# Performance work log

Hardware: AMD Instinct MI355X
Metric: run time of the kernel (lower is better)

## Reference

```python
import jax, jax.numpy as jnp
import numpy as np
import math

D_MODEL = 1024
H = 16
D_K = D_MODEL // H          # 64
D_HALF = D_MODEL // 2       # 512
DH = D_HALF // H            # 32 (half head dim for q/k)
B, S = 2, 1024
LAMBDA_INIT = 0.8 - 0.6 * math.exp(-0.3 * (1 - 1))  # layer_index=1 -> 0.2


def setup_inputs() -> dict:
    key = jax.random.key(0)
    ks = jax.random.split(key, 20)
    def lin(kk, fan_in, fan_out):
        lim = 1.0 / math.sqrt(fan_in)
        kw, kb = jax.random.split(kk)
        W = jax.random.uniform(kw, (fan_in, fan_out), jnp.float32, -lim, lim)
        b = jax.random.uniform(kb, (fan_out,), jnp.float32, -lim, lim)
        return W, b
    Wq1, bq1 = lin(ks[0], D_MODEL, D_HALF)
    Wq2, bq2 = lin(ks[1], D_MODEL, D_HALF)
    Wk1, bk1 = lin(ks[2], D_MODEL, D_HALF)
    Wk2, bk2 = lin(ks[3], D_MODEL, D_HALF)
    Wv, bv = lin(ks[4], D_MODEL, D_MODEL)
    Wo, bo = lin(ks[5], D_MODEL, D_MODEL)
    q = jax.random.normal(ks[6], (B, S, D_MODEL), jnp.float32)
    k = jax.random.normal(ks[7], (B, S, D_MODEL), jnp.float32)
    v = jax.random.normal(ks[8], (B, S, D_MODEL), jnp.float32)
    # causal 0/1 mask, already 4-D [B,1,S,S]
    mask = jnp.broadcast_to(jnp.tril(jnp.ones((S, S), jnp.int32)), (B, 1, S, S))
    # small random lambda scalars (torch inits to 0 -> degenerate gradients)
    lq1 = jax.random.normal(ks[9], (1,), jnp.float32) * 0.1
    lk1 = jax.random.normal(ks[10], (1,), jnp.float32) * 0.1
    lq2 = jax.random.normal(ks[11], (1,), jnp.float32) * 0.1
    lk2 = jax.random.normal(ks[12], (1,), jnp.float32) * 0.1
    return dict(q=q, k=k, v=v, mask=mask,
                Wq1=Wq1, bq1=bq1, Wq2=Wq2, bq2=bq2,
                Wk1=Wk1, bk1=bk1, Wk2=Wk2, bk2=bk2,
                Wv=Wv, bv=bv, Wo=Wo, bo=bo,
                lq1=lq1, lk1=lk1, lq2=lq2, lk2=lk2)


def reference(q, k, v, mask, Wq1, bq1, Wq2, bq2, Wk1, bk1, Wk2, bk2,
              Wv, bv, Wo, bo, lq1, lk1, lq2, lk2):
    b, sq, _ = q.shape
    sk = k.shape[1]
    # projections, reshaped to [B, S, H, head_dim]
    q1 = (q @ Wq1 + bq1).reshape(b, sq, H, DH)
    q2 = (q @ Wq2 + bq2).reshape(b, sq, H, DH)
    k1 = (k @ Wk1 + bk1).reshape(b, sk, H, DH)
    k2 = (k @ Wk2 + bk2).reshape(b, sk, H, DH)
    vv = (v @ Wv + bv).reshape(b, sk, H, D_K)
    lam = jnp.exp(lq1 * lk1) - jnp.exp(lq2 * lk2) + LAMBDA_INIT  # shape (1,)
    scale = 1.0 / math.sqrt(D_K)
    s1 = jnp.einsum('bqhd,bkhd->bhqk', q1, k1) * scale
    s2 = jnp.einsum('bqhd,bkhd->bhqk', q2, k2) * scale
    neg = jnp.float32(-1e9)
    keep = mask != 0  # [B,1,Sq,Sk], broadcasts over heads
    s1 = jnp.where(keep, s1, neg)
    s2 = jnp.where(keep, s2, neg)
    a1 = jax.nn.softmax(s1, axis=-1)
    a2 = jax.nn.softmax(s2, axis=-1)
    diff = a1 - lam[0] * a2  # dropout p=0.0 -> identity
    out = jnp.einsum('bhqk,bkhd->bqhd', diff, vv).reshape(b, sq, D_MODEL)
    return out @ Wo + bo
```

## Files before the change

### kernel.cpp

```cpp
#include <hip/hip_runtime.h>
#include <hip/hip_bf16.h>
#include <cstdint>
#include <cstddef>

typedef __attribute__((ext_vector_type(8))) short short8;
typedef __attribute__((ext_vector_type(4))) float floatx4;

#define B_ 2
#define S_ 1024
#define H_ 16
#define DM_ 1024
#define DHALF_ 512
#define DH_ 32
#define DK_ 64
#define LAMBDA_INIT_ 0.2f
#define SCALE_ 0.125f
#define M_INIT_ -1.0e4f
#define MASK_NEG_ -1.0e9f

static __device__ __forceinline__ unsigned short f2bf(float f) {
  uint32_t u = __float_as_uint(f);
  uint32_t r = (u + 0x7fffu + ((u >> 16) & 1u)) >> 16;
  return (unsigned short)r;
}

static __device__ __forceinline__ uint32_t pkbf(float a, float b) {
  __hip_bfloat162 h = __float22bfloat162_rn(make_float2(a, b));
  return *reinterpret_cast<uint32_t*>(&h);
}

static __device__ __forceinline__ void gload16(const void* g, void* l) {
  __builtin_amdgcn_global_load_lds(
      (const __attribute__((address_space(1))) uint32_t*)g,
      (__attribute__((address_space(3))) uint32_t*)l, 16, 0, 0);
}

__global__ __launch_bounds__(256) void prep_kernel(
    const float* __restrict__ q, const float* __restrict__ k, const float* __restrict__ v,
    const float* __restrict__ Wq1, const float* __restrict__ Wq2,
    const float* __restrict__ Wk1, const float* __restrict__ Wk2,
    const float* __restrict__ Wv, const float* __restrict__ Wo,
    const float* __restrict__ bq1, const float* __restrict__ bq2,
    const float* __restrict__ bk1, const float* __restrict__ bk2,
    unsigned short* __restrict__ WqT, unsigned short* __restrict__ WkT,
    unsigned short* __restrict__ WvT, unsigned short* __restrict__ WoT,
    unsigned short* __restrict__ qbf, unsigned short* __restrict__ kbf,
    unsigned short* __restrict__ vbf,
    float* __restrict__ biasQ, float* __restrict__ biasK)
{
  __shared__ float tile[64][65];
  const int bid = blockIdx.x;
  const int tid = threadIdx.x;
  if (bid < 1024) {
    const float* W; unsigned short* WT; int ncols, n_off, local;
    if (bid < 128)      { W = Wq1; WT = WqT; ncols = 512;  n_off = 0;   local = bid; }
    else if (bid < 256) { W = Wq2; WT = WqT; ncols = 512;  n_off = 512; local = bid - 128; }
    else if (bid < 384) { W = Wk1; WT = WkT; ncols = 512;  n_off = 0;   local = bid - 256; }
    else if (bid < 512) { W = Wk2; WT = WkT; ncols = 512;  n_off = 512; local = bid - 384; }
    else if (bid < 768) { W = Wv;  WT = WvT; ncols = 1024; n_off = 0;   local = bid - 512; }
    else                { W = Wo;  WT = WoT; ncols = 1024; n_off = 0;   local = bid - 768; }
    const int ntiles = ncols >> 6;
    const int n0 = (local % ntiles) * 64;
    const int k0 = (local / ntiles) * 64;
#pragma unroll
    for (int i = 0; i < 4; ++i) {
      int idx = tid + 256 * i;
      int r = idx >> 4, c4 = idx & 15;
      float4 val = *reinterpret_cast<const float4*>(W + (size_t)(k0 + r) * ncols + n0 + c4 * 4);
      tile[r][c4 * 4 + 0] = val.x; tile[r][c4 * 4 + 1] = val.y;
      tile[r][c4 * 4 + 2] = val.z; tile[r][c4 * 4 + 3] = val.w;
    }
    __syncthreads();
#pragma unroll
    for (int i = 0; i < 2; ++i) {
      int G = tid + 256 * i;
      int n = G >> 3, g = G & 7;
      short8 o;
#pragma unroll
      for (int j = 0; j < 8; ++j) o[j] = (short)f2bf(tile[g * 8 + j][n]);
      *reinterpret_cast<short8*>(WT + (size_t)(n_off + n0 + n) * 1024 + k0 + g * 8) = o;
    }
  } else if (bid < 4096) {
    int local = bid - 1024;
    int t = local >> 10;
    int i = local & 1023;
    const float* src = (t == 0) ? q : ((t == 1) ? k : v);
    unsigned short* dst = (t == 0) ? qbf : ((t == 1) ? kbf : vbf);
    const int base = i * 2048 + tid * 8;
    float4 a = *reinterpret_cast<const float4*>(src + base);
    float4 b2 = *reinterpret_cast<const float4*>(src + base + 4);
    short8 o;
    o[0] = (short)f2bf(a.x);  o[1] = (short)f2bf(a.y);
    o[2] = (short)f2bf(a.z);  o[3] = (short)f2bf(a.w);
    o[4] = (short)f2bf(b2.x); o[5] = (short)f2bf(b2.y);
    o[6] = (short)f2bf(b2.z); o[7] = (short)f2bf(b2.w);
    *reinterpret_cast<short8*>(dst + base) = o;
  } else {
#pragma unroll
    for (int j = 0; j < 4; ++j) {
      int i = j * 256 + tid;
      biasQ[i] = (i < 512) ? bq1[i] : bq2[i - 512];
      biasK[i] = (i < 512) ? bk1[i] : bk2[i - 512];
    }
  }
}

template<int ROWS>
static __device__ __forceinline__ void stage_rows(
    const unsigned short* __restrict__ G, int row0, int kk0,
    unsigned short* L, int tid)
{
#pragma unroll
  for (int i = 0; i < ROWS / 32; ++i) {
    const int o = i * 4096 + tid * 16;
    const int r = o >> 7;
    const int c = ((o >> 4) & 7) ^ (r & 7);
    gload16(G + (size_t)(row0 + r) * 1024 + kk0 + c * 8, L + (o >> 1));
  }
}

template<int BM, int BN>
static __device__ __forceinline__ void gemm_mainloop(
    const unsigned short* __restrict__ A, const unsigned short* __restrict__ BT,
    int m0, int n0,
    unsigned short* As0, unsigned short* As1,
    unsigned short* Bs0, unsigned short* Bs1,
    floatx4 (&acc)[BM / 32][BN / 32])
{
  constexpr int MT = BM / 32, NT = BN / 32;
  const int tid = threadIdx.x;
  const int lane = tid & 63;
  const int l15 = lane & 15, hi = lane >> 4;
  const int wid = tid >> 6;
  const int wr = wid >> 1, wc = wid & 1;

  stage_rows<BM>(A, m0, 0, As0, tid);
  stage_rows<BN>(BT, n0, 0, Bs0, tid);
  __syncthreads();

  for (int ks = 0; ks < 16; ++ks) {
    unsigned short* Ac = (ks & 1) ? As1 : As0;
    unsigned short* Bc = (ks & 1) ? Bs1 : Bs0;
    unsigned short* An = (ks & 1) ? As0 : As1;
    unsigned short* Bn = (ks & 1) ? Bs0 : Bs1;
    if (ks < 15) {
      stage_rows<BM>(A, m0, (ks + 1) * 64, An, tid);
      stage_rows<BN>(BT, n0, (ks + 1) * 64, Bn, tid);
    }
#pragma unroll
    for (int kk = 0; kk < 2; ++kk) {
      short8 af[MT], bf[NT];
#pragma unroll
      for (int mt = 0; mt < MT; ++mt) {
        const int r = wr * (BM / 2) + mt * 16 + l15;
        af[mt] = *reinterpret_cast<const short8*>(Ac + r * 64 + (((kk * 4 + hi) ^ (r & 7)) << 3));
      }
#pragma unroll
      for (int nt = 0; nt < NT; ++nt) {
        const int r = wc * (BN / 2) + nt * 16 + l15;
        bf[nt] = *reinterpret_cast<const short8*>(Bc + r * 64 + (((kk * 4 + hi) ^ (r & 7)) << 3));
      }
#pragma unroll
      for (int mt = 0; mt < MT; ++mt)
#pragma unroll
        for (int nt = 0; nt < NT; ++nt)
          acc[mt][nt] = __builtin_amdgcn_mfma_f32_16x16x32_bf16(af[mt], bf[nt], acc[mt][nt], 0, 0, 0);
    }
    __syncthreads();
  }
}

__global__ __launch_bounds__(256) void proj_gemm_kernel(
    const unsigned short* __restrict__ qbf, const unsigned short* __restrict__ kbf,
    const unsigned short* __restrict__ vbf,
    const unsigned short* __restrict__ WqT, const unsigned short* __restrict__ WkT,
    const unsigned short* __restrict__ WvT,
    const float* __restrict__ biasQ, const float* __restrict__ biasK,
    const float* __restrict__ bv,
    unsigned short* __restrict__ q12b, unsigned short* __restrict__ k12b,
    unsigned short* __restrict__ vvT)
{
  __shared__ unsigned short As[2][128 * 64];
  __shared__ unsigned short Bs[2][64 * 64];
  const int z = blockIdx.z;
  const unsigned short* A = (z == 0) ? qbf : ((z == 1) ? kbf : vbf);
  const unsigned short* BT = (z == 0) ? WqT : ((z == 1) ? WkT : WvT);
  const float* bias = (z == 0) ? biasQ : ((z == 1) ? biasK : bv);
  const int n0 = blockIdx.x * 64;
  const int m0 = blockIdx.y * 128;
  const int lane = threadIdx.x & 63, wid = threadIdx.x >> 6;
  const int l15 = lane & 15, hi = lane >> 4;
  const int wr = wid >> 1, wc = wid & 1;

  floatx4 acc[4][2];
#pragma unroll
  for (int a = 0; a < 4; ++a)
#pragma unroll
    for (int c = 0; c < 2; ++c) acc[a][c] = (floatx4){0.f, 0.f, 0.f, 0.f};

  gemm_mainloop<128, 64>(A, BT, m0, n0, As[0], As[1], Bs[0], Bs[1], acc);

#pragma unroll
  for (int nt = 0; nt < 2; ++nt) {
    const int n = n0 + wc * 32 + nt * 16 + l15;
    const float bn = bias[n];
#pragma unroll
    for (int mt = 0; mt < 4; ++mt) {
      const int mrow = m0 + wr * 64 + mt * 16 + 4 * hi;
      if (z < 2) {
        unsigned short* dst = (z == 0 ? q12b : k12b);
#pragma unroll
        for (int r = 0; r < 4; ++r)
          dst[(size_t)(mrow + r) * 1024 + n] = f2bf(acc[mt][nt][r] + bn);
      } else {
        const int bb = mrow >> 10, ss = mrow & 1023;
        const int hh = n >> 6, dd = n & 63;
        float v0 = acc[mt][nt][0] + bn, v1 = acc[mt][nt][1] + bn;
        float v2 = acc[mt][nt][2] + bn, v3 = acc[mt][nt][3] + bn;
        uint2 pk;
        pk.x = pkbf(v0, v1);
        pk.y = pkbf(v2, v3);
        *reinterpret_cast<uint2*>(vvT + ((size_t)(bb * 16 + hh) * 64 + dd) * 1024 + ss) = pk;
      }
    }
  }
}

__global__ __launch_bounds__(256) void out_gemm_kernel(
    const unsigned short* __restrict__ Ab, const unsigned short* __restrict__ BT,
    const float* __restrict__ bias, float* __restrict__ out)
{
  __shared__ unsigned short As[2][64 * 64];
  __shared__ unsigned short Bs[2][64 * 64];
  const int n0 = blockIdx.x * 64;
  const int m0 = blockIdx.y * 64;
  const int lane = threadIdx.x & 63, wid = threadIdx.x >> 6;
  const int l15 = lane & 15, hi = lane >> 4;
  const int wr = wid >> 1, wc = wid & 1;

  floatx4 acc[2][2];
#pragma unroll
  for (int a = 0; a < 2; ++a)
#pragma unroll
    for (int c = 0; c < 2; ++c) acc[a][c] = (floatx4){0.f, 0.f, 0.f, 0.f};

  gemm_mainloop<64, 64>(Ab, BT, m0, n0, As[0], As[1], Bs[0], Bs[1], acc);

#pragma unroll
  for (int nt = 0; nt < 2; ++nt) {
    const int n = n0 + wc * 32 + nt * 16 + l15;
    const float bn = bias[n];
#pragma unroll
    for (int mt = 0; mt < 2; ++mt) {
      const int mrow = m0 + wr * 32 + mt * 16 + 4 * hi;
#pragma unroll
      for (int r = 0; r < 4; ++r)
        out[(size_t)(mrow + r) * 1024 + n] = acc[mt][nt][r] + bn;
    }
  }
}

#define STAGE_KV(kbase_, bi_)                                                  \
  {                                                                            \
    const size_t krow0_ = (size_t)(b * S_ + (kbase_));                         \
    _Pragma("unroll")                                                          \
    for (int i_ = 0; i_ < 2; ++i_) {                                           \
      const int o_ = i_ * 8192 + tid * 16;              \
      const int kr_ = o_ >> 7;                         \
      const int kc_ = ((o_ >> 4) & 7) ^ (kr_ & 7);                             \
      const unsigned short* ks_ = (kc_ < 4)                                    \
          ? (k12b + (krow0_ + kr_) * DM_ + h * DH_ + kc_ * 8)                  \
          : (k12b + (krow0_ + kr_) * DM_ + DHALF_ + h * DH_ + (kc_ - 4) * 8);  \
      gload16(ks_, &Kt[bi_][0] + (o_ >> 1));                                   \
      const int vr_ = o_ >> 8;                          \
      const int vc_ = ((o_ >> 4) & 15) ^ (vr_ & 15);                           \
      gload16(vvT + (vrow0 + vr_) * (size_t)S_ + (kbase_) + vc_ * 8,           \
              &Vt[bi_][0] + (o_ >> 1));                                        \
    }                                                                          \
  }

__global__ __launch_bounds__(512) void diff_attn_kernel(
    const unsigned short* __restrict__ q12b, const unsigned short* __restrict__ k12b,
    const unsigned short* __restrict__ vvT, unsigned short* __restrict__ attn,
    const float* __restrict__ lq1, const float* __restrict__ lk1,
    const float* __restrict__ lq2, const float* __restrict__ lk2)
{
  __shared__ unsigned short Kt[2][128 * 64];
  __shared__ unsigned short Vt[2][64 * 128];
  __shared__ unsigned short Pl[8][16 * 64];

  const int tid = threadIdx.x;
  const int lane = tid & 63, wid = tid >> 6;
  const int st = wid & 1;
  const int qw = wid >> 1;
  const int l15 = lane & 15, hi = lane >> 4;

  const int idx = blockIdx.x;
  const int hf = idx >> 8;
  const int pk = idx & 255;
  const int h = pk & 15;
  const int b = (pk >> 4) & 1;
  const int j = pk >> 5;
  const int qblk = hf ? (15 - j) : j;

  const int qbase = qblk * 64 + qw * 16;
  const float lam = __expf(lq1[0] * lk1[0]) - __expf(lq2[0] * lk2[0]) + LAMBDA_INIT_;
  const size_t vrow0 = (size_t)(b * H_ + h) * DK_;

  const size_t qrow = (size_t)(b * S_ + qbase + l15) * DM_;
  const short8 qf = *reinterpret_cast<const short8*>(
      q12b + qrow + st * DHALF_ + h * DH_ + hi * 8);

  floatx4 acc[4];
#pragma unroll
  for (int dt = 0; dt < 4; ++dt) acc[dt] = (floatx4){0.f, 0.f, 0.f, 0.f};
  float m = M_INIT_, l = 0.f;

  unsigned short* P = &Pl[wid][0];

  const int ntiles = (qblk >> 1) + 1;
  STAGE_KV(0, 0);
  __syncthreads();

  for (int kb = 0; kb < ntiles; ++kb) {
    const int cur = kb & 1;
    const int kbase = kb * 128;
    if (kb + 1 < ntiles) STAGE_KV(kbase + 128, cur ^ 1);

    floatx4 s[8];
    const floatx4 zz = (floatx4){0.f, 0.f, 0.f, 0.f};
    __builtin_amdgcn_s_setprio(1);
#pragma unroll
    for (int t = 0; t < 8; ++t) {
      const int r = 16 * t + l15;
      short8 kf = *reinterpret_cast<const short8*>(
          &Kt[cur][0] + r * 64 + (((hi + 4 * st) ^ (r & 7)) << 3));
      s[t] = __builtin_amdgcn_mfma_f32_16x16x32_bf16(kf, qf, zz, 0, 0, 0);
    }
    __builtin_amdgcn_s_setprio(0);

    if (kb == ntiles - 1) {
      const int qg = qbase + l15;
#pragma unroll
      for (int t = 0; t < 8; ++t) {
#pragma unroll
        for (int e = 0; e < 4; ++e) {
          const int kg = kbase + 16 * t + 4 * hi + e;
          if (kg > qg) s[t][e] = MASK_NEG_;
        }
      }
    }

    float tm;
    {
      float x = fmaxf(fmaxf(s[0][0], s[0][1]), fmaxf(s[0][2], s[0][3]));
#pragma unroll
      for (int t = 1; t < 8; ++t)
        x = fmaxf(x, fmaxf(fmaxf(s[t][0], s[t][1]), fmaxf(s[t][2], s[t][3])));
      tm = x;
    }
    tm = fmaxf(tm, __shfl_xor(tm, 16));
    tm = fmaxf(tm, __shfl_xor(tm, 32));

    const float nm = fmaxf(m, tm);
    const float sc = __expf((m - nm) * SCALE_);
    m = nm;
#pragma unroll
    for (int dt = 0; dt < 4; ++dt) acc[dt] *= sc;

    float rs = 0.f;
#pragma unroll
    for (int half = 0; half < 2; ++half) {
#pragma unroll
      for (int tt = 0; tt < 4; ++tt) {
        const int t = half * 4 + tt;
        float p0 = __expf((s[t][0] - m) * SCALE_);
        float p1 = __expf((s[t][1] - m) * SCALE_);
        float p2 = __expf((s[t][2] - m) * SCALE_);
        float p3 = __expf((s[t][3] - m) * SCALE_);
        rs += (p0 + p1) + (p2 + p3);
        const int idx2 = l15 * 64 + (((2 * tt + (hi >> 1)) ^ (l15 & 7)) << 3) + ((hi & 1) << 2);
        uint2 w1; w1.x = pkbf(p0, p1); w1.y = pkbf(p2, p3);
        *reinterpret_cast<uint2*>(P + idx2) = w1;
      }
      __builtin_amdgcn_s_setprio(1);
#pragma unroll
      for (int kc = 0; kc < 2; ++kc) {
        short8 pf = *reinterpret_cast<const short8*>(
            P + l15 * 64 + (((hi + 4 * kc) ^ (l15 & 7)) << 3));
#pragma unroll
        for (int dt = 0; dt < 4; ++dt) {
          const int d = dt * 16 + l15;
          short8 vf = *reinterpret_cast<const short8*>(
              &Vt[cur][0] + d * 128 + (((hi + 4 * (2 * half + kc)) ^ (d & 15)) << 3));
          acc[dt] = __builtin_amdgcn_mfma_f32_16x16x32_bf16(vf, pf, acc[dt], 0, 0, 0);
        }
      }
      __builtin_amdgcn_s_setprio(0);
    }
    rs += __shfl_xor(rs, 16);
    rs += __shfl_xor(rs, 32);
    l = l * sc + rs;

    __syncthreads();
  }

  float* Os = reinterpret_cast<float*>(&Kt[0][0]);
  if (st == 1) {
    const float inv2 = lam / l;
    float* dstp = Os + qw * (16 * 68) + l15 * 68;
#pragma unroll
    for (int dt = 0; dt < 4; ++dt) {
#pragma unroll
      for (int e = 0; e < 4; ++e)
        dstp[dt * 16 + 4 * hi + e] = acc[dt][e] * inv2;
    }
  }
  __syncthreads();
  if (st == 0) {
    const float inv1 = 1.0f / l;
    const float* srcp = Os + qw * (16 * 68) + l15 * 68;
    const int qg = qbase + l15;
    unsigned short* op = attn + (size_t)(b * S_ + qg) * DM_ + h * DK_;
#pragma unroll
    for (int dt = 0; dt < 4; ++dt) {
      float o0 = acc[dt][0] * inv1 - srcp[dt * 16 + 4 * hi + 0];
      float o1 = acc[dt][1] * inv1 - srcp[dt * 16 + 4 * hi + 1];
      float o2 = acc[dt][2] * inv1 - srcp[dt * 16 + 4 * hi + 2];
      float o3 = acc[dt][3] * inv1 - srcp[dt * 16 + 4 * hi + 3];
      uint2 pkv;
      pkv.x = pkbf(o0, o1);
      pkv.y = pkbf(o2, o3);
      *reinterpret_cast<uint2*>(op + dt * 16 + 4 * hi) = pkv;
    }
  }
}

extern "C" void kernel_launch(void* const* d_in, const int* in_sizes, int n_in,
                              void* d_out, int out_size, void* d_ws, size_t ws_size,
                              hipStream_t stream)
{
  const float* q   = (const float*)d_in[0];
  const float* k   = (const float*)d_in[1];
  const float* v   = (const float*)d_in[2];
  const float* Wq1 = (const float*)d_in[4];
  const float* bq1 = (const float*)d_in[5];
  const float* Wq2 = (const float*)d_in[6];
  const float* bq2 = (const float*)d_in[7];
  const float* Wk1 = (const float*)d_in[8];
  const float* bk1 = (const float*)d_in[9];
  const float* Wk2 = (const float*)d_in[10];
  const float* bk2 = (const float*)d_in[11];
  const float* Wv  = (const float*)d_in[12];
  const float* bv  = (const float*)d_in[13];
  const float* Wo  = (const float*)d_in[14];
  const float* bo  = (const float*)d_in[15];
  const float* lq1 = (const float*)d_in[16];
  const float* lk1 = (const float*)d_in[17];
  const float* lq2 = (const float*)d_in[18];
  const float* lk2 = (const float*)d_in[19];
  float* out = (float*)d_out;

  uint8_t* w = (uint8_t*)d_ws;
  unsigned short* WqT  = (unsigned short*)w; w += (size_t)2 * 1024 * 1024;
  unsigned short* WkT  = (unsigned short*)w; w += (size_t)2 * 1024 * 1024;
  unsigned short* WvT  = (unsigned short*)w; w += (size_t)2 * 1024 * 1024;
  unsigned short* WoT  = (unsigned short*)w; w += (size_t)2 * 1024 * 1024;
  unsigned short* qbf  = (unsigned short*)w; w += (size_t)4 * 1024 * 1024;
  unsigned short* kbf  = (unsigned short*)w; w += (size_t)4 * 1024 * 1024;
  unsigned short* vbf  = (unsigned short*)w; w += (size_t)4 * 1024 * 1024;
  unsigned short* q12b = (unsigned short*)w; w += (size_t)4 * 1024 * 1024;
  unsigned short* k12b = (unsigned short*)w; w += (size_t)4 * 1024 * 1024;
  unsigned short* vvT  = (unsigned short*)w; w += (size_t)4 * 1024 * 1024;
  float* biasQ = (float*)w; w += 4096;
  float* biasK = (float*)w; w += 4096;
  unsigned short* attnb = qbf;

  dim3 blk(256);
  hipLaunchKernelGGL(prep_kernel, dim3(4097), blk, 0, stream,
                     q, k, v, Wq1, Wq2, Wk1, Wk2, Wv, Wo,
                     bq1, bq2, bk1, bk2,
                     WqT, WkT, WvT, WoT, qbf, kbf, vbf, biasQ, biasK);

  hipLaunchKernelGGL(proj_gemm_kernel, dim3(16, 16, 3), blk, 0, stream,
                     qbf, kbf, vbf, WqT, WkT, WvT, biasQ, biasK, bv,
                     q12b, k12b, vvT);

  hipLaunchKernelGGL(diff_attn_kernel, dim3(512), dim3(512), 0, stream,
                     q12b, k12b, vvT, attnb, lq1, lk1, lq2, lk2);

  hipLaunchKernelGGL(out_gemm_kernel, dim3(16, 32), blk, 0, stream,
                     attnb, WoT, bo, out);
}
```

Baseline: 71.46 us.

## Load K/V fragments directly from global memory instead of LDS staging

Drops the double-buffered LDS staging of K and V tiles and the per-tile block barrier. Each wave now reads its MFMA K and V fragments straight from global memory (through the caches). The LDS footprint shrinks, and launch bounds now request 4 blocks per CU for higher occupancy. In exchange, the waves of a block no longer share their K/V loads, so redundant global/L2 traffic goes up. Load latency is also no longer hidden by prefetching a tile ahead.

Result: slower. 98.66 us (+38.1%).

```diff
diff --git a/kernel.cpp b/kernel.cpp
--- a/kernel.cpp
+++ b/kernel.cpp
@@ -260,34 +260,14 @@
   }
 }
 
-#define STAGE_KV(kbase_, bi_)                                                  \
-  {                                                                            \
-    const size_t krow0_ = (size_t)(b * S_ + (kbase_));                         \
-    _Pragma("unroll")                                                          \
-    for (int i_ = 0; i_ < 2; ++i_) {                                           \
-      const int o_ = i_ * 8192 + tid * 16;              \
-      const int kr_ = o_ >> 7;                         \
-      const int kc_ = ((o_ >> 4) & 7) ^ (kr_ & 7);                             \
-      const unsigned short* ks_ = (kc_ < 4)                                    \
-          ? (k12b + (krow0_ + kr_) * DM_ + h * DH_ + kc_ * 8)                  \
-          : (k12b + (krow0_ + kr_) * DM_ + DHALF_ + h * DH_ + (kc_ - 4) * 8);  \
-      gload16(ks_, &Kt[bi_][0] + (o_ >> 1));                                   \
-      const int vr_ = o_ >> 8;                          \
-      const int vc_ = ((o_ >> 4) & 15) ^ (vr_ & 15);                           \
-      gload16(vvT + (vrow0 + vr_) * (size_t)S_ + (kbase_) + vc_ * 8,           \
-              &Vt[bi_][0] + (o_ >> 1));                                        \
-    }                                                                          \
-  }
-
-__global__ __launch_bounds__(512) void diff_attn_kernel(
+__global__ __launch_bounds__(512, 4) void diff_attn_kernel(
     const unsigned short* __restrict__ q12b, const unsigned short* __restrict__ k12b,
     const unsigned short* __restrict__ vvT, unsigned short* __restrict__ attn,
     const float* __restrict__ lq1, const float* __restrict__ lk1,
     const float* __restrict__ lq2, const float* __restrict__ lk2)
 {
-  __shared__ unsigned short Kt[2][128 * 64];
-  __shared__ unsigned short Vt[2][64 * 128];
   __shared__ unsigned short Pl[8][16 * 64];
+  __shared__ float Os[4][16][68];
 
   const int tid = threadIdx.x;
   const int lane = tid & 63, wid = tid >> 6;
@@ -305,12 +285,15 @@
 
   const int qbase = qblk * 64 + qw * 16;
   const float lam = __expf(lq1[0] * lk1[0]) - __expf(lq2[0] * lk2[0]) + LAMBDA_INIT_;
-  const size_t vrow0 = (size_t)(b * H_ + h) * DK_;
 
   const size_t qrow = (size_t)(b * S_ + qbase + l15) * DM_;
   const short8 qf = *reinterpret_cast<const short8*>(
       q12b + qrow + st * DHALF_ + h * DH_ + hi * 8);
 
+  const unsigned short* kp = k12b + ((size_t)(b * S_ + l15)) * DM_ +
+                             st * DHALF_ + h * DH_ + hi * 8;
+  const unsigned short* vp = vvT + ((size_t)(b * H_ + h) * DK_ + l15) * S_ + hi * 8;
+
   floatx4 acc[4];
 #pragma unroll
   for (int dt = 0; dt < 4; ++dt) acc[dt] = (floatx4){0.f, 0.f, 0.f, 0.f};
@@ -319,22 +302,16 @@
   unsigned short* P = &Pl[wid][0];
 
   const int ntiles = (qblk >> 1) + 1;
-  STAGE_KV(0, 0);
-  __syncthreads();
 
   for (int kb = 0; kb < ntiles; ++kb) {
-    const int cur = kb & 1;
     const int kbase = kb * 128;
-    if (kb + 1 < ntiles) STAGE_KV(kbase + 128, cur ^ 1);
 
     floatx4 s[8];
     const floatx4 zz = (floatx4){0.f, 0.f, 0.f, 0.f};
     __builtin_amdgcn_s_setprio(1);
 #pragma unroll
     for (int t = 0; t < 8; ++t) {
-      const int r = 16 * t + l15;
-      short8 kf = *reinterpret_cast<const short8*>(
-          &Kt[cur][0] + r * 64 + (((hi + 4 * st) ^ (r & 7)) << 3));
+      short8 kf = *reinterpret_cast<const short8*>(kp + (size_t)(kbase + 16 * t) * DM_);
       s[t] = __builtin_amdgcn_mfma_f32_16x16x32_bf16(kf, qf, zz, 0, 0, 0);
     }
     __builtin_amdgcn_s_setprio(0);
@@ -390,9 +367,8 @@
             P + l15 * 64 + (((hi + 4 * kc) ^ (l15 & 7)) << 3));
 #pragma unroll
         for (int dt = 0; dt < 4; ++dt) {
-          const int d = dt * 16 + l15;
           short8 vf = *reinterpret_cast<const short8*>(
-              &Vt[cur][0] + d * 128 + (((hi + 4 * (2 * half + kc)) ^ (d & 15)) << 3));
+              vp + (size_t)(dt * 16) * S_ + kbase + (2 * half + kc) * 32);
           acc[dt] = __builtin_amdgcn_mfma_f32_16x16x32_bf16(vf, pf, acc[dt], 0, 0, 0);
         }
       }
@@ -401,14 +377,11 @@
     rs += __shfl_xor(rs, 16);
     rs += __shfl_xor(rs, 32);
     l = l * sc + rs;
-
-    __syncthreads();
-  }
-
-  float* Os = reinterpret_cast<float*>(&Kt[0][0]);
+  }
+
   if (st == 1) {
     const float inv2 = lam / l;
-    float* dstp = Os + qw * (16 * 68) + l15 * 68;
+    float* dstp = &Os[qw][l15][0];
 #pragma unroll
     for (int dt = 0; dt < 4; ++dt) {
 #pragma unroll
@@ -419,7 +392,7 @@
   __syncthreads();
   if (st == 0) {
     const float inv1 = 1.0f / l;
-    const float* srcp = Os + qw * (16 * 68) + l15 * 68;
+    const float* srcp = &Os[qw][l15][0];
     const int qg = qbase + l15;
     unsigned short* op = attn + (size_t)(b * S_ + qg) * DM_ + h * DK_;
 #pragma unroll
```

## Add lazy softmax rescaling and XCD-aware block-to-head mapping in attention

Applied to the files above, without the earlier changes.

Online softmax now rescales the accumulator and the running sum only when some lane's new tile max exceeds the running max by a threshold; otherwise it reuses the stale max. This removes the per-tile accumulator rescale and its exp. Separately, block indices are remapped so that blocks sharing a (batch, head) land on the same XCD, which should improve L2 reuse of K/V. The lazy rescale assumes exp of at most 8 units of headroom stays within fp32 and bf16 range.

Result: no change. 70.40 us (-1.5%).

```diff
diff --git a/kernel.cpp b/kernel.cpp
--- a/kernel.cpp
+++ b/kernel.cpp
@@ -295,12 +295,15 @@
   const int qw = wid >> 1;
   const int l15 = lane & 15, hi = lane >> 4;
 
-  const int idx = blockIdx.x;
-  const int hf = idx >> 8;
-  const int pk = idx & 255;
-  const int h = pk & 15;
-  const int b = (pk >> 4) & 1;
-  const int j = pk >> 5;
+  const int bid = blockIdx.x;
+  const int xcd = bid & 7;
+  const int i = bid >> 3;
+  const int g = xcd * 4 + (i & 3);
+  const int member = i >> 2;
+  const int h = g & 15;
+  const int b = g >> 4;
+  const int j = member & 7;
+  const int hf = member >> 3;
   const int qblk = hf ? (15 - j) : j;
 
   const int qbase = qblk * 64 + qw * 16;
@@ -362,25 +365,44 @@
     tm = fmaxf(tm, __shfl_xor(tm, 16));
     tm = fmaxf(tm, __shfl_xor(tm, 32));
 
-    const float nm = fmaxf(m, tm);
-    const float sc = __expf((m - nm) * SCALE_);
-    m = nm;
-#pragma unroll
-    for (int dt = 0; dt < 4; ++dt) acc[dt] *= sc;
+    if (kb == 0) {
+      m = tm;
+#pragma unroll
+      for (int t = 0; t < 8; ++t)
+#pragma unroll
+        for (int e = 0; e < 4; ++e)
+          s[t][e] = __expf((s[t][e] - m) * SCALE_);
+    } else {
+#pragma unroll
+      for (int t = 0; t < 8; ++t)
+#pragma unroll
+        for (int e = 0; e < 4; ++e)
+          s[t][e] = __expf((s[t][e] - m) * SCALE_);
+      if (__any(tm > m + 64.0f)) {
+        const float nm = fmaxf(m, tm);
+        const float sc = __expf((m - nm) * SCALE_);
+#pragma unroll
+        for (int t = 0; t < 8; ++t)
+#pragma unroll
+          for (int e = 0; e < 4; ++e) s[t][e] *= sc;
+#pragma unroll
+        for (int dt = 0; dt < 4; ++dt) acc[dt] *= sc;
+        l *= sc;
+        m = nm;
+      }
+    }
 
     float rs = 0.f;
+#pragma unroll
+    for (int t = 0; t < 8; ++t) rs += (s[t][0] + s[t][1]) + (s[t][2] + s[t][3]);
+
 #pragma unroll
     for (int half = 0; half < 2; ++half) {
 #pragma unroll
       for (int tt = 0; tt < 4; ++tt) {
         const int t = half * 4 + tt;
-        float p0 = __expf((s[t][0] - m) * SCALE_);
-        float p1 = __expf((s[t][1] - m) * SCALE_);
-        float p2 = __expf((s[t][2] - m) * SCALE_);
-        float p3 = __expf((s[t][3] - m) * SCALE_);
-        rs += (p0 + p1) + (p2 + p3);
         const int idx2 = l15 * 64 + (((2 * tt + (hi >> 1)) ^ (l15 & 7)) << 3) + ((hi & 1) << 2);
-        uint2 w1; w1.x = pkbf(p0, p1); w1.y = pkbf(p2, p3);
+        uint2 w1; w1.x = pkbf(s[t][0], s[t][1]); w1.y = pkbf(s[t][2], s[t][3]);
         *reinterpret_cast<uint2*>(P + idx2) = w1;
       }
       __builtin_amdgcn_s_setprio(1);
@@ -398,9 +420,10 @@
       }
       __builtin_amdgcn_s_setprio(0);
     }
+
     rs += __shfl_xor(rs, 16);
     rs += __shfl_xor(rs, 32);
-    l = l * sc + rs;
+    l += rs;
 
     __syncthreads();
   }
```
